# Performance work log

Measured on AMD Instinct MI355X. Metric: run time of the kernel, lower is better.

The kernel has to match this reference:

```python
import jax, jax.numpy as jnp
import numpy as np

B, N, D = 8, 2048, 768
K, H, G = 256, 12, 4
DH = D // H          # 64
EPS = 1e-12


def grouped_pointwise(x, w):
    """Grouped Conv1d with kernel_size=1, no bias.
    x: (b, n, d); w: (g, out_per_g, in_per_g) [torch weight (d, d/g, 1) reshaped].
    """
    b, n, d = x.shape
    g = w.shape[0]
    xg = x.reshape(b, n, g, d // g)
    return jnp.einsum('bngi,goi->bngo', xg, w).reshape(b, n, d)


def setup_inputs() -> dict:
    key = jax.random.key(0)
    ks = jax.random.split(key, 8)
    std_conv = 1.0 / np.sqrt(D // G)   # torch conv default ~ U(-sqrt(1/fan_in), ...)
    std_pk = 1.0 / np.sqrt(K)          # init_ uses last dim of (seq_len, k_dim)
    std_lin = 1.0 / np.sqrt(D)
    return {
        'input_embedding': jax.random.normal(ks[0], (B, N, D), jnp.float32),
        'wq': jax.random.uniform(ks[1], (G, D // G, D // G), jnp.float32, -std_conv, std_conv),
        'wk': jax.random.uniform(ks[2], (G, D // G, D // G), jnp.float32, -std_conv, std_conv),
        'project_k': jax.random.uniform(ks[3], (N, K), jnp.float32, -std_pk, std_pk),
        'w_out': jax.random.uniform(ks[4], (D, D), jnp.float32, -std_lin, std_lin),
        'b_out': jax.random.uniform(ks[5], (D,), jnp.float32, -std_lin, std_lin),
        'gamma': jnp.ones((D,), jnp.float32),
        'beta': jnp.zeros((D,), jnp.float32),
    }


def reference(input_embedding, wq, wk, project_k, w_out, b_out, gamma, beta):
    x = input_embedding                       # (b, n, d)
    b, n, d = x.shape

    queries = grouped_pointwise(x, wq)        # (b, n, d)
    k_raw = grouped_pointwise(x, wk)          # (b, n, d)  (key conv)
    k_proj = jnp.einsum('bnd,nk->bkd', k_raw, project_k)   # (b, K, d)

    # Faithful replication of: keys.permute(0,2,1).view(b, K, h, dh)
    # (memory-reinterpreting reshape of the (b, d, K) layout)
    keys = jnp.transpose(k_proj, (0, 2, 1)).reshape(b, K, H, DH)
    keys = jnp.transpose(keys, (0, 2, 1, 3))                # (b, h, K, dh)

    # values also come from the key conv (self.value unused in source forward)
    values = k_proj.reshape(b, K, H, DH).transpose(0, 2, 1, 3)   # (b, h, K, dh)
    q = queries.reshape(b, n, H, DH).transpose(0, 2, 1, 3)       # (b, h, n, dh)

    dots = jnp.einsum('bhnd,bhkd->bhnk', q, keys) / np.sqrt(DH)
    attn = jax.nn.softmax(dots, axis=-1)      # dropout = identity (eval)
    ctx = jnp.einsum('bhnk,bhkd->bhnd', attn, values)
    ctx = ctx.transpose(0, 2, 1, 3).reshape(b, n, d)

    out = ctx @ w_out.T + b_out               # nn.Linear
    y = x + out                               # residual
    mu = jnp.mean(y, axis=-1, keepdims=True)
    var = jnp.mean((y - mu) ** 2, axis=-1, keepdims=True)
    return (y - mu) / jnp.sqrt(var + EPS) * gamma + beta
```

## Files before the change

### kernel.cpp

```cpp
#include <hip/hip_runtime.h>
#include <hip/hip_bf16.h>

typedef short short8 __attribute__((ext_vector_type(8)));
typedef short short4v __attribute__((ext_vector_type(4)));
typedef int i32x4 __attribute__((ext_vector_type(4)));
typedef float f32x4 __attribute__((ext_vector_type(4)));

#define MFMA(a, b, c) __builtin_amdgcn_mfma_f32_16x16x32_bf16((a), (b), (c), 0, 0, 0)

__device__ __forceinline__ short f2bf(float f) {
  unsigned u = __builtin_bit_cast(unsigned, f);
  unsigned r = u + 0x7FFFu + ((u >> 16) & 1u);
  return (short)(r >> 16);
}

__device__ __forceinline__ float bf2f(short s) {
  unsigned u = ((unsigned)(unsigned short)s) << 16;
  return __builtin_bit_cast(float, u);
}

__device__ __forceinline__ short8 cvt8(float4 a, float4 b) {
  short8 t;
  t[0] = f2bf(a.x); t[1] = f2bf(a.y); t[2] = f2bf(a.z); t[3] = f2bf(a.w);
  t[4] = f2bf(b.x); t[5] = f2bf(b.y); t[6] = f2bf(b.z); t[7] = f2bf(b.w);
  return t;
}

__global__ __launch_bounds__(256) void k_prep(
    const float* __restrict__ wq, const float* __restrict__ wk,
    const float* __restrict__ wout, const float* __restrict__ pk,
    short* __restrict__ wqb, short* __restrict__ wkb,
    short* __restrict__ woutb, short* __restrict__ pkT)
{
  int idx = blockIdx.x * 256 + threadIdx.x;
  if (idx < 147456) { wqb[idx] = f2bf(wq[idx]); wkb[idx] = f2bf(wk[idx]); }
  if (idx < 589824) { woutb[idx] = f2bf(wout[idx]); }
  if (idx < 524288) {
    int n = idx >> 8, k = idx & 255;
    pkT[(size_t)k * 2048 + n] = f2bf(pk[idx]);
  }
}

__global__ __launch_bounds__(512, 8) void k_conv(
    const float* __restrict__ x, const short* __restrict__ wqb,
    short* __restrict__ qo, short* __restrict__ xbT)
{
  __shared__ __align__(16) short Xs[64 * 192];
  const int tid = threadIdx.x, lane = tid & 63, w = tid >> 6;
  const int g = blockIdx.y;
  const int m0 = blockIdx.x * 64;
  const int lrow = lane & 15, g4 = lane >> 4, lk8 = g4 * 8;
  const int wr16 = (w >> 1) * 16, wcol = (w & 1) * 96;

  {
    const int r = tid >> 3, j8 = tid & 7;
    const int sw = (r ^ (r >> 3)) & 7;
    const float* src = x + (size_t)(m0 + r) * 768 + g * 192 + j8 * 24;
#pragma unroll
    for (int i = 0; i < 3; i++) {
      float4 v0 = *(const float4*)(src + i * 8);
      float4 v1 = *(const float4*)(src + i * 8 + 4);
      int o = j8 * 3 + i;
      *(short8*)&Xs[r * 192 + ((o ^ sw) << 3)] = cvt8(v0, v1);
    }
  }
  __syncthreads();

  f32x4 acc[6];
#pragma unroll
  for (int cf = 0; cf < 6; cf++) acc[cf] = (f32x4)0.f;

  const int arow = wr16 + lrow;
  const int asw = (arow ^ (arow >> 3)) & 7;
#pragma unroll
  for (int s = 0; s < 6; s++) {
    const int ob = s * 4 + g4;
    short8 a0 = *(const short8*)&Xs[arow * 192 + ((ob ^ asw) << 3)];
#pragma unroll
    for (int cf = 0; cf < 6; cf++) {
      short8 bb = *(const short8*)(wqb + ((size_t)g * 192 + wcol + cf * 16 + lrow) * 192 + s * 32 + lk8);
      acc[cf] = MFMA(a0, bb, acc[cf]);
    }
  }

#pragma unroll
  for (int cf = 0; cf < 6; cf++)
#pragma unroll
    for (int j = 0; j < 4; j++) {
      int m = m0 + wr16 + g4 * 4 + j;
      qo[(size_t)m * 768 + g * 192 + wcol + cf * 16 + lrow] = f2bf(acc[cf][j]);
    }

  {
    const int b = m0 >> 11, n0 = m0 & 2047;
    const int t = tid & 255, set = tid >> 8;
    const int el = t >> 3, oct = t & 7;
#pragma unroll
    for (int ec = 0; ec < 3; ec++) {
      const int c = (set * 3 + ec) * 32 + el;
      const int o = c >> 3, ci = c & 7;
      short8 v;
#pragma unroll
      for (int u = 0; u < 8; u++) {
        const int n = oct * 8 + u;
        v[u] = Xs[n * 192 + (((o ^ (u ^ oct)) << 3)) + ci];
      }
      *(short8*)(xbT + ((size_t)b * 768 + g * 192 + c) * 2048 + n0 + oct * 8) = v;
    }
  }
}

__global__ __launch_bounds__(512, 4) void k_xproj(
    const short* __restrict__ pkT, const short* __restrict__ xbT,
    float* __restrict__ xproj)
{
  __shared__ __align__(16) short A2[2][64][72];
  __shared__ __align__(16) short B2[2][64][72];
  const int tid = threadIdx.x, lane = tid & 63, w = tid >> 6;
  const int f = blockIdx.x;
  const int xcd = f & 7, rem = f >> 3;
  const int k2t4 = rem & 3, eb8 = rem >> 2;
  const int e_b = eb8 * 8 + xcd;
  const int k2t = k2t4 * 64;
  const int et = (e_b % 12) * 64, b = e_b / 12;
  const int lrow = lane & 15, g4 = lane >> 4, lk8 = g4 * 8;
  const int wa = (w & 3) * 16, wb = (w >> 2) * 32;

  const int r = tid >> 3, c8 = tid & 7;
  const short* aSrc = pkT + (size_t)(k2t + r) * 2048 + c8 * 8;
  const short* bSrc = xbT + ((size_t)b * 768 + et + r) * 2048 + c8 * 8;

  {
    short8 gA = *(const short8*)aSrc;
    short8 gB = *(const short8*)bSrc;
    *(short8*)&A2[0][r][c8 * 8] = gA;
    *(short8*)&B2[0][r][c8 * 8] = gB;
  }
  __syncthreads();

  f32x4 acc[2];
  acc[0] = (f32x4)0.f; acc[1] = (f32x4)0.f;

  short8 gA, gB;
#pragma unroll 2
  for (int t = 0; t < 32; ++t) {
    const int cur = t & 1;
    if (t < 31) {
      gA = *(const short8*)(aSrc + (t + 1) * 64);
      gB = *(const short8*)(bSrc + (t + 1) * 64);
    }
    short8 af0 = *(const short8*)&A2[cur][wa + lrow][lk8];
    short8 af1 = *(const short8*)&A2[cur][wa + lrow][32 + lk8];
    short8 bf00 = *(const short8*)&B2[cur][wb + lrow][lk8];
    short8 bf01 = *(const short8*)&B2[cur][wb + lrow][32 + lk8];
    short8 bf10 = *(const short8*)&B2[cur][wb + 16 + lrow][lk8];
    short8 bf11 = *(const short8*)&B2[cur][wb + 16 + lrow][32 + lk8];
    acc[0] = MFMA(af0, bf00, acc[0]);
    acc[0] = MFMA(af1, bf01, acc[0]);
    acc[1] = MFMA(af0, bf10, acc[1]);
    acc[1] = MFMA(af1, bf11, acc[1]);
    if (t < 31) {
      *(short8*)&A2[cur ^ 1][r][c8 * 8] = gA;
      *(short8*)&B2[cur ^ 1][r][c8 * 8] = gB;
    }
    __syncthreads();
  }

  float* dst = xproj + ((size_t)b * 256 + k2t + wa) * 768 + et + wb;
#pragma unroll
  for (int cf = 0; cf < 2; cf++)
#pragma unroll
    for (int j = 0; j < 4; j++)
      dst[(size_t)(g4 * 4 + j) * 768 + cf * 16 + lrow] = acc[cf][j];
}

__global__ __launch_bounds__(256) void k_kconv(
    float* xpio, const short* __restrict__ wkb)
{
  const int tid = threadIdx.x, lane = tid & 63, w = tid >> 6;
  const int rt = blockIdx.x * 64, g = blockIdx.y, b = blockIdx.z;
  const int wr = (w >> 1) * 32, wcol = (w & 1) * 96;
  const int lrow = lane & 15, g4 = lane >> 4, lk8 = (lane >> 4) * 8;

  f32x4 acc[2][6];
#pragma unroll
  for (int mi = 0; mi < 2; mi++)
#pragma unroll
    for (int cf = 0; cf < 6; cf++) acc[mi][cf] = (f32x4)0.f;

#pragma unroll
  for (int s = 0; s < 6; s++) {
    int k0 = s * 32;
    short8 af[2];
#pragma unroll
    for (int mi = 0; mi < 2; mi++) {
      const float* ap = xpio + ((size_t)b * 256 + rt + wr + mi * 16 + lrow) * 768
                        + g * 192 + k0 + lk8;
      float4 f0 = *(const float4*)ap;
      float4 f1 = *(const float4*)(ap + 4);
      af[mi] = cvt8(f0, f1);
    }
#pragma unroll
    for (int cf = 0; cf < 6; cf++) {
      short8 bb = *(const short8*)(wkb + ((size_t)g * 192 + wcol + cf * 16 + lrow) * 192 + k0 + lk8);
      acc[0][cf] = MFMA(af[0], bb, acc[0][cf]);
      acc[1][cf] = MFMA(af[1], bb, acc[1][cf]);
    }
  }
  __syncthreads();
#pragma unroll
  for (int mi = 0; mi < 2; mi++)
#pragma unroll
    for (int cf = 0; cf < 6; cf++)
#pragma unroll
      for (int j = 0; j < 4; j++) {
        int k2 = rt + wr + mi * 16 + g4 * 4 + j;
        xpio[((size_t)b * 256 + k2) * 768 + g * 192 + wcol + cf * 16 + lrow] =
            acc[mi][cf][j];
      }
}

__global__ __launch_bounds__(256) void k_gather(
    const float* __restrict__ kp, short* __restrict__ Kb, short* __restrict__ Vb)
{
  const int h = blockIdx.x, b = blockIdx.y;
  const int bh = b * 12 + h;
  const int tid = threadIdx.x;
  const float* kpb = kp + (size_t)b * 196608;
  {
    const int kb4 = (h & 3) * 64, doff = h >> 2;
    const int dh = tid & 63, kq = tid >> 6;
    const float* row = kpb + (size_t)(kb4 + dh) * 768 + doff;
    short* dst = Kb + (size_t)bh * 18432 + dh;
#pragma unroll 8
    for (int i = 0; i < 64; i++) {
      int k2 = kq * 64 + i;
      dst[(size_t)k2 * 72] = f2bf(row[3 * k2]);
    }
  }
  {
    short* dst = Vb + (size_t)bh * 16384;
#pragma unroll
    for (int i = 0; i < 8; i++) {
      int oct = tid + 256 * i;
      int k2h = oct >> 6, dh = oct & 63;
      short8 v;
#pragma unroll
      for (int u = 0; u < 8; u++)
        v[u] = f2bf(kpb[(size_t)(k2h * 8 + u) * 768 + h * 64 + dh]);
      *(short8*)&dst[oct * 8] = v;
    }
  }
}

__global__ __launch_bounds__(512, 4) void k_attn(
    const short* __restrict__ qws, const short* __restrict__ Kb,
    const short* __restrict__ Vb, short* __restrict__ ctx)
{
  __shared__ __align__(16) short Kls[18432];
  __shared__ __align__(16) short Vls[16384];
  const int tid = threadIdx.x, lane = tid & 63, w = tid >> 6;
  const int n0 = blockIdx.x * 128;
  const int h = blockIdx.y, b = blockIdx.z;
  const int bh = b * 12 + h;

  {
    const short8* gk = (const short8*)(Kb + (size_t)bh * 18432);
    short8* lk = (short8*)Kls;
#pragma unroll
    for (int i = 0; i < 4; i++) lk[tid + 512 * i] = gk[tid + 512 * i];
    if (tid < 256) lk[tid + 2048] = gk[tid + 2048];
    const short8* gv = (const short8*)(Vb + (size_t)bh * 16384);
    short8* lv = (short8*)Vls;
#pragma unroll
    for (int i = 0; i < 4; i++) lv[tid + 512 * i] = gv[tid + 512 * i];
  }
  const int lrow = lane & 15, g = lane >> 4, lk8 = g * 8;
  const int nrow = n0 + w * 16;
  const short* qp = qws + ((size_t)b * 2048 + nrow + lrow) * 768 + h * 64;
  short8 bq0 = *(const short8*)(qp + lk8);
  short8 bq1 = *(const short8*)(qp + 32 + lk8);
  __syncthreads();

  f32x4 s[16];
#pragma unroll
  for (int fc = 0; fc < 16; fc++) s[fc] = (f32x4)0.f;
  __builtin_amdgcn_s_setprio(1);
#pragma unroll
  for (int fc = 0; fc < 16; fc++) {
    short8 ak0 = *(const short8*)&Kls[(fc * 16 + lrow) * 72 + lk8];
    short8 ak1 = *(const short8*)&Kls[(fc * 16 + lrow) * 72 + 32 + lk8];
    s[fc] = MFMA(ak0, bq0, s[fc]);
    s[fc] = MFMA(ak1, bq1, s[fc]);
  }
  __builtin_amdgcn_s_setprio(0);

  float mx = -3.0e38f;
#pragma unroll
  for (int fc = 0; fc < 16; fc++)
#pragma unroll
    for (int j = 0; j < 4; j++) mx = fmaxf(mx, s[fc][j]);
  mx = fmaxf(mx, __shfl_xor(mx, 16));
  mx = fmaxf(mx, __shfl_xor(mx, 32));
  float sum = 0.f;
#pragma unroll
  for (int fc = 0; fc < 16; fc++)
#pragma unroll
    for (int j = 0; j < 4; j++) {
      float e = __expf(0.125f * (s[fc][j] - mx));
      s[fc][j] = e; sum += e;
    }
  sum += __shfl_xor(sum, 16);
  sum += __shfl_xor(sum, 32);
  float inv = 1.f / sum;

  unsigned pku[16][2];
#pragma unroll
  for (int fc = 0; fc < 16; fc++) {
    pku[fc][0] = (unsigned)(unsigned short)f2bf(s[fc][0] * inv)
               | ((unsigned)(unsigned short)f2bf(s[fc][1] * inv) << 16);
    pku[fc][1] = (unsigned)(unsigned short)f2bf(s[fc][2] * inv)
               | ((unsigned)(unsigned short)f2bf(s[fc][3] * inv) << 16);
  }

  f32x4 o[4];
#pragma unroll
  for (int fd = 0; fd < 4; fd++) o[fd] = (f32x4)0.f;
  const int L0 = ((lane & 16) << 1) + lrow;
  const int L1 = L0 + 16;
  const bool hi = (lane >= 32);
  __builtin_amdgcn_s_setprio(1);
#pragma unroll
  for (int t = 0; t < 8; t++) {
    unsigned a0 = (unsigned)__shfl((int)pku[2 * t][0], L0);
    unsigned a1 = (unsigned)__shfl((int)pku[2 * t][1], L0);
    unsigned a2 = (unsigned)__shfl((int)pku[2 * t][0], L1);
    unsigned a3 = (unsigned)__shfl((int)pku[2 * t][1], L1);
    unsigned c0 = (unsigned)__shfl((int)pku[2 * t + 1][0], L0);
    unsigned c1 = (unsigned)__shfl((int)pku[2 * t + 1][1], L0);
    unsigned c2 = (unsigned)__shfl((int)pku[2 * t + 1][0], L1);
    unsigned c3 = (unsigned)__shfl((int)pku[2 * t + 1][1], L1);
    i32x4 bi = { (int)(hi ? c0 : a0), (int)(hi ? c1 : a1),
                 (int)(hi ? c2 : a2), (int)(hi ? c3 : a3) };
    short8 bfrag = __builtin_bit_cast(short8, bi);
#pragma unroll
    for (int fd = 0; fd < 4; fd++) {
      short8 av = *(const short8*)&Vls[((t * 4 + g) * 64 + fd * 16 + lrow) * 8];
      o[fd] = MFMA(av, bfrag, o[fd]);
    }
  }
  __builtin_amdgcn_s_setprio(0);
#pragma unroll
  for (int fd = 0; fd < 4; fd++) {
    short4v st;
#pragma unroll
    for (int j = 0; j < 4; j++) st[j] = f2bf(o[fd][j]);
    *(short4v*)&ctx[((size_t)b * 2048 + n0 + w * 16 + lrow) * 768
                    + h * 64 + fd * 16 + 4 * g] = st;
  }
}

__global__ __launch_bounds__(512, 4) void k_gemm_y(
    const short* __restrict__ ctx, const short* __restrict__ woutb,
    const float* __restrict__ bout, const float* __restrict__ x,
    short* __restrict__ ybf)
{
  __shared__ __align__(16) short As[2][128][40];
  __shared__ __align__(16) short Bs[2][128][40];
  const int tid = threadIdx.x, lane = tid & 63, w = tid >> 6;
  const int f = blockIdx.x;
  const int xcd = f & 7, rem = f >> 3;
  const int mi_l = rem / 6, ni = rem % 6;
  const int m0 = (xcd * 16 + mi_l) * 128;
  const int n0 = ni * 128;
  const int lrow = lane & 15, g4 = lane >> 4, lk8 = g4 * 8;
  const int wr2 = (w >> 2) * 64, wc4 = (w & 3) * 32;

  const int r = tid >> 2, c8 = (tid & 3) * 8;
  const short* aSrc = ctx + (size_t)(m0 + r) * 768 + c8;
  const short* bSrc = woutb + (size_t)(n0 + r) * 768 + c8;

  {
    short8 gA = *(const short8*)aSrc;
    short8 gB = *(const short8*)bSrc;
    *(short8*)&As[0][r][c8] = gA;
    *(short8*)&Bs[0][r][c8] = gB;
  }
  __syncthreads();

  f32x4 acc[4][2];
#pragma unroll
  for (int rf = 0; rf < 4; rf++)
#pragma unroll
    for (int cf = 0; cf < 2; cf++) acc[rf][cf] = (f32x4)0.f;

  short8 gA, gB;
#pragma unroll 2
  for (int t = 0; t < 24; ++t) {
    const int cur = t & 1;
    if (t < 23) {
      gA = *(const short8*)(aSrc + (t + 1) * 32);
      gB = *(const short8*)(bSrc + (t + 1) * 32);
    }
    short8 af[4], bf[2];
#pragma unroll
    for (int rf = 0; rf < 4; rf++)
      af[rf] = *(const short8*)&As[cur][wr2 + rf * 16 + lrow][lk8];
#pragma unroll
    for (int cf = 0; cf < 2; cf++)
      bf[cf] = *(const short8*)&Bs[cur][wc4 + cf * 16 + lrow][lk8];
#pragma unroll
    for (int cf = 0; cf < 2; cf++)
#pragma unroll
      for (int rf = 0; rf < 4; rf++)
        acc[rf][cf] = MFMA(af[rf], bf[cf], acc[rf][cf]);
    if (t < 23) {
      *(short8*)&As[cur ^ 1][r][c8] = gA;
      *(short8*)&Bs[cur ^ 1][r][c8] = gB;
    }
    __syncthreads();
  }

  float cB[2];
#pragma unroll
  for (int cf = 0; cf < 2; cf++) cB[cf] = bout[n0 + wc4 + cf * 16 + lrow];
#pragma unroll
  for (int rf = 0; rf < 4; rf++)
#pragma unroll
    for (int j = 0; j < 4; j++) {
      int row = m0 + wr2 + rf * 16 + g4 * 4 + j;
      const float* xr = x + (size_t)row * 768 + n0 + wc4;
      short* yr = ybf + (size_t)row * 768 + n0 + wc4;
#pragma unroll
      for (int cf = 0; cf < 2; cf++)
        yr[cf * 16 + lrow] = f2bf(acc[rf][cf][j] + cB[cf] + xr[cf * 16 + lrow]);
    }
}

__global__ __launch_bounds__(256) void k_ln(
    const short* __restrict__ ybf, const float* __restrict__ gamma,
    const float* __restrict__ beta, float* __restrict__ out)
{
  const int tid = threadIdx.x, lane = tid & 63, w = tid >> 6;
  const int half = lane >> 5, l5 = lane & 31;
  const int row = blockIdx.x * 8 + w * 2 + half;
  const short* yr = ybf + (size_t)row * 768;

  float v[24];
  float s1 = 0.f, s2 = 0.f;
#pragma unroll
  for (int j = 0; j < 3; j++) {
    short8 p = *(const short8*)(yr + (l5 + 32 * j) * 8);
#pragma unroll
    for (int u = 0; u < 8; u++) {
      float fv = bf2f(p[u]);
      v[j * 8 + u] = fv;
      s1 += fv; s2 += fv * fv;
    }
  }
  s1 += __shfl_xor(s1, 1, 32);  s2 += __shfl_xor(s2, 1, 32);
  s1 += __shfl_xor(s1, 2, 32);  s2 += __shfl_xor(s2, 2, 32);
  s1 += __shfl_xor(s1, 4, 32);  s2 += __shfl_xor(s2, 4, 32);
  s1 += __shfl_xor(s1, 8, 32);  s2 += __shfl_xor(s2, 8, 32);
  s1 += __shfl_xor(s1, 16, 32); s2 += __shfl_xor(s2, 16, 32);
  float mean = s1 * (1.f / 768.f);
  float var = s2 * (1.f / 768.f) - mean * mean;
  float rstd = rsqrtf(var + 1e-12f);

  float* orow = out + (size_t)row * 768;
#pragma unroll
  for (int j = 0; j < 3; j++) {
    int c0 = (l5 + 32 * j) * 8;
    float4 o0, o1;
    o0.x = (v[j*8+0] - mean) * rstd * gamma[c0+0] + beta[c0+0];
    o0.y = (v[j*8+1] - mean) * rstd * gamma[c0+1] + beta[c0+1];
    o0.z = (v[j*8+2] - mean) * rstd * gamma[c0+2] + beta[c0+2];
    o0.w = (v[j*8+3] - mean) * rstd * gamma[c0+3] + beta[c0+3];
    o1.x = (v[j*8+4] - mean) * rstd * gamma[c0+4] + beta[c0+4];
    o1.y = (v[j*8+5] - mean) * rstd * gamma[c0+5] + beta[c0+5];
    o1.z = (v[j*8+6] - mean) * rstd * gamma[c0+6] + beta[c0+6];
    o1.w = (v[j*8+7] - mean) * rstd * gamma[c0+7] + beta[c0+7];
    *(float4*)(orow + c0) = o0;
    *(float4*)(orow + c0 + 4) = o1;
  }
}

extern "C" void kernel_launch(void* const* d_in, const int* in_sizes, int n_in,
                              void* d_out, int out_size, void* d_ws, size_t ws_size,
                              hipStream_t stream)
{
  const float* x     = (const float*)d_in[0];
  const float* wq    = (const float*)d_in[1];
  const float* wk    = (const float*)d_in[2];
  const float* pk    = (const float*)d_in[3];
  const float* wout  = (const float*)d_in[4];
  const float* bout  = (const float*)d_in[5];
  const float* gamma = (const float*)d_in[6];
  const float* beta  = (const float*)d_in[7];
  float* out = (float*)d_out;

  char* ws = (char*)d_ws;
  short* qbf   = (short*)(ws + 0);
  short* xbT   = (short*)(ws + 25165824);
  float* kpbuf = (float*)(ws + 50331648);
  short* wqb   = (short*)(ws + 56623104);
  short* wkb   = (short*)(ws + 56918016);
  short* woutb = (short*)(ws + 57212928);
  short* pkT   = (short*)(ws + 58392576);
  if (ws_size < 59441152) return;
  short* ctx = (short*)xbT;
  short* ybf = qbf;

  short* Kb = (short*)d_out;
  short* Vb = Kb + 96 * 18432;

  k_prep<<<2304, 256, 0, stream>>>(wq, wk, wout, pk, wqb, wkb, woutb, pkT);
  k_conv<<<dim3(256, 4), 512, 0, stream>>>(x, wqb, qbf, xbT);
  k_xproj<<<384, 512, 0, stream>>>(pkT, xbT, kpbuf);
  k_kconv<<<dim3(4, 4, 8), 256, 0, stream>>>(kpbuf, wkb);
  k_gather<<<dim3(12, 8), 256, 0, stream>>>(kpbuf, Kb, Vb);
  k_attn<<<dim3(16, 12, 8), 512, 0, stream>>>(qbf, Kb, Vb, ctx);
  k_gemm_y<<<768, 512, 0, stream>>>(ctx, woutb, bout, x, ybf);
  k_ln<<<2048, 256, 0, stream>>>(ybf, gamma, beta, out);
}
```

Before: 179.9 us.

## Loop k_conv over all groups per block with double-buffered shared-memory prefetch

The pointwise-conv kernel changes from one 512-thread block per (64-row tile, group) to one 256-thread block per 32-row tile that loops over all four groups. While the MFMA work and the transposed xbT stores run for the current group from one shared buffer, the next group's fp32 input slice is loaded into registers and then converted into a second shared buffer. The aim is to hide global load latency behind compute and cut block launch overhead. The cost is a smaller block with fewer waves, extra barriers per group, and higher register pressure from the prefetch registers.

```diff
diff --git a/kernel.cpp b/kernel.cpp
--- a/kernel.cpp
+++ b/kernel.cpp
@@ -41,71 +41,90 @@
   }
 }
 
-__global__ __launch_bounds__(512, 8) void k_conv(
+__global__ __launch_bounds__(256, 4) void k_conv(
     const float* __restrict__ x, const short* __restrict__ wqb,
     short* __restrict__ qo, short* __restrict__ xbT)
 {
-  __shared__ __align__(16) short Xs[64 * 192];
+  __shared__ __align__(16) short Xs[2][32 * 192];
   const int tid = threadIdx.x, lane = tid & 63, w = tid >> 6;
-  const int g = blockIdx.y;
-  const int m0 = blockIdx.x * 64;
+  const int m0 = blockIdx.x * 32;
   const int lrow = lane & 15, g4 = lane >> 4, lk8 = g4 * 8;
-  const int wr16 = (w >> 1) * 16, wcol = (w & 1) * 96;
-
-  {
-    const int r = tid >> 3, j8 = tid & 7;
-    const int sw = (r ^ (r >> 3)) & 7;
-    const float* src = x + (size_t)(m0 + r) * 768 + g * 192 + j8 * 24;
-#pragma unroll
-    for (int i = 0; i < 3; i++) {
-      float4 v0 = *(const float4*)(src + i * 8);
-      float4 v1 = *(const float4*)(src + i * 8 + 4);
-      int o = j8 * 3 + i;
-      *(short8*)&Xs[r * 192 + ((o ^ sw) << 3)] = cvt8(v0, v1);
-    }
+  const int wr = (w >> 1) * 16, wcol = (w & 1) * 96;
+
+  const int r = tid >> 3, cb = (tid & 3 + 0, (tid & 7) * 24);
+  const int sw = (r ^ (r >> 3)) & 7;
+  const float* srcRow = x + (size_t)(m0 + r) * 768 + cb;
+
+#pragma unroll
+  for (int i = 0; i < 3; i++) {
+    float4 v0 = *(const float4*)(srcRow + i * 8);
+    float4 v1 = *(const float4*)(srcRow + i * 8 + 4);
+    int o = (cb >> 3) + i;
+    *(short8*)&Xs[0][r * 192 + ((o ^ sw) << 3)] = cvt8(v0, v1);
   }
   __syncthreads();
 
-  f32x4 acc[6];
-#pragma unroll
-  for (int cf = 0; cf < 6; cf++) acc[cf] = (f32x4)0.f;
-
-  const int arow = wr16 + lrow;
-  const int asw = (arow ^ (arow >> 3)) & 7;
-#pragma unroll
-  for (int s = 0; s < 6; s++) {
-    const int ob = s * 4 + g4;
-    short8 a0 = *(const short8*)&Xs[arow * 192 + ((ob ^ asw) << 3)];
-#pragma unroll
-    for (int cf = 0; cf < 6; cf++) {
-      short8 bb = *(const short8*)(wqb + ((size_t)g * 192 + wcol + cf * 16 + lrow) * 192 + s * 32 + lk8);
-      acc[cf] = MFMA(a0, bb, acc[cf]);
-    }
-  }
-
-#pragma unroll
-  for (int cf = 0; cf < 6; cf++)
-#pragma unroll
-    for (int j = 0; j < 4; j++) {
-      int m = m0 + wr16 + g4 * 4 + j;
-      qo[(size_t)m * 768 + g * 192 + wcol + cf * 16 + lrow] = f2bf(acc[cf][j]);
-    }
-
-  {
-    const int b = m0 >> 11, n0 = m0 & 2047;
-    const int t = tid & 255, set = tid >> 8;
-    const int el = t >> 3, oct = t & 7;
+  const int row0 = wr + lrow;
+  const int sw0 = (row0 ^ (row0 >> 3)) & 7;
+  const int b = m0 >> 11, n0 = m0 & 2047;
+  const int oct = tid & 3, el = tid >> 2;
+
+#pragma unroll
+  for (int g = 0; g < 4; ++g) {
+    const int cur = g & 1;
+    float4 pf[6];
+    if (g < 3) {
+      const float* src = srcRow + (g + 1) * 192;
+#pragma unroll
+      for (int i = 0; i < 3; i++) {
+        pf[2 * i]     = *(const float4*)(src + i * 8);
+        pf[2 * i + 1] = *(const float4*)(src + i * 8 + 4);
+      }
+    }
+
+    f32x4 acc[6];
+#pragma unroll
+    for (int cf = 0; cf < 6; cf++) acc[cf] = (f32x4)0.f;
+#pragma unroll
+    for (int s = 0; s < 6; s++) {
+      const int ob = s * 4 + g4;
+      short8 a0 = *(const short8*)&Xs[cur][row0 * 192 + ((ob ^ sw0) << 3)];
+#pragma unroll
+      for (int cf = 0; cf < 6; cf++) {
+        short8 bb = *(const short8*)(wqb + ((size_t)g * 192 + wcol + cf * 16 + lrow) * 192 + s * 32 + lk8);
+        acc[cf] = MFMA(a0, bb, acc[cf]);
+      }
+    }
+
+#pragma unroll
+    for (int cf = 0; cf < 6; cf++)
+#pragma unroll
+      for (int j = 0; j < 4; j++) {
+        int m = m0 + wr + g4 * 4 + j;
+        qo[(size_t)m * 768 + g * 192 + wcol + cf * 16 + lrow] = f2bf(acc[cf][j]);
+      }
+
 #pragma unroll
     for (int ec = 0; ec < 3; ec++) {
-      const int c = (set * 3 + ec) * 32 + el;
+      const int c = ec * 64 + el;
       const int o = c >> 3, ci = c & 7;
       short8 v;
 #pragma unroll
       for (int u = 0; u < 8; u++) {
         const int n = oct * 8 + u;
-        v[u] = Xs[n * 192 + (((o ^ (u ^ oct)) << 3)) + ci];
+        v[u] = Xs[cur][n * 192 + ((o ^ ((n ^ (n >> 3)) & 7)) << 3) + ci];
       }
       *(short8*)(xbT + ((size_t)b * 768 + g * 192 + c) * 2048 + n0 + oct * 8) = v;
+    }
+
+    __syncthreads();
+    if (g < 3) {
+#pragma unroll
+      for (int i = 0; i < 3; i++) {
+        int o = (cb >> 3) + i;
+        *(short8*)&Xs[cur ^ 1][r * 192 + ((o ^ sw) << 3)] = cvt8(pf[2 * i], pf[2 * i + 1]);
+      }
+      __syncthreads();
     }
   }
 }
@@ -515,7 +534,7 @@
   short* Vb = Kb + 96 * 18432;
 
   k_prep<<<2304, 256, 0, stream>>>(wq, wk, wout, pk, wqb, wkb, woutb, pkT);
-  k_conv<<<dim3(256, 4), 512, 0, stream>>>(x, wqb, qbf, xbT);
+  k_conv<<<512, 256, 0, stream>>>(x, wqb, qbf, xbT);
   k_xproj<<<384, 512, 0, stream>>>(pkT, xbT, kpbuf);
   k_kconv<<<dim3(4, 4, 8), 256, 0, stream>>>(kpbuf, wkb);
   k_gather<<<dim3(12, 8), 256, 0, stream>>>(kpbuf, Kb, Vb);
```

Measured after the change: 180.1 us. No clear change (+0.1%).
